# Kernel tuning notes

Measured on AMD Instinct MI355X. Metric: run time of the kernel, lower is better.

## Reference

```python
import jax, jax.numpy as jnp
import numpy as np

C_IN, C_OUT = 64, 32
SD, RFF = 2, 16
RF = 0.05          # receptive_field percentile
TEMP = 1.0
EPS = 1e-8
RFF_STD = 6.0


def setup_inputs() -> dict:
    key = jax.random.key(0)
    ks = jax.random.split(key, 10)
    B_, T, V, Q = 2, 4, 2048, 512
    x = jax.random.normal(ks[0], (B_, T, V, C_IN), dtype=jnp.float32)
    pos = jax.random.uniform(ks[1], (V, SD), dtype=jnp.float32)
    query_pos = jax.random.uniform(ks[2], (Q, SD), dtype=jnp.float32)
    s = 1.0 / np.sqrt(C_IN)
    W_lin = jax.random.uniform(ks[3], (C_IN, C_IN), minval=-s, maxval=s, dtype=jnp.float32)
    b_lin = jax.random.uniform(ks[4], (C_IN,), minval=-s, maxval=s, dtype=jnp.float32)
    Bmat = RFF_STD * jax.random.normal(ks[5], (SD, RFF), dtype=jnp.float32)
    s1 = 1.0 / np.sqrt(32)
    W1 = jax.random.uniform(ks[6], (32, 32), minval=-s1, maxval=s1, dtype=jnp.float32)
    b1 = jax.random.uniform(ks[7], (32,), minval=-s1, maxval=s1, dtype=jnp.float32)
    W2 = jax.random.uniform(ks[8], (C_IN * C_OUT, 32), minval=-s1, maxval=s1, dtype=jnp.float32)
    sf = np.sqrt(3.0 / C_IN)
    filt = jax.random.uniform(ks[9], (C_IN * C_OUT,), minval=-sf, maxval=sf, dtype=jnp.float32)
    bias = jnp.zeros((C_OUT,), dtype=jnp.float32)
    return {"x": x, "pos": pos, "query_pos": query_pos, "W_lin": W_lin, "b_lin": b_lin,
            "Bmat": Bmat, "W1": W1, "b1": b1, "W2": W2, "filt": filt, "bias": bias}


def reference(x, pos, query_pos, W_lin, b_lin, Bmat, W1, b1, W2, filt, bias):
    # pairwise periodic displacement / squared distance
    dist = query_pos[:, None, :] - pos[None, :, :]            # (Q, V, 2)
    dist = (dist + 0.5) % 1.0 - 0.5                           # periodic wrap
    edist = jnp.sum(dist ** 2, axis=-1)                       # (Q, V)
    # quantile threshold -> max neighbourhood size (eager, data-dependent like torch)
    thr = jnp.quantile(edist, RF, axis=-1, keepdims=True)     # linear interpolation, as torch
    K = int(jnp.max(jnp.sum(edist <= thr, axis=-1)))
    _, ind = jax.lax.top_k(-edist, K)                         # (Q, K) nearest neighbours
    # gather per-query neighbour displacements / distances
    d_g = jnp.take_along_axis(dist, ind[..., None], axis=1)   # (Q, K, 2)
    e_g = jnp.take_along_axis(edist, ind, axis=1)[..., None]  # (Q, K, 1)
    e_g = e_g - jnp.min(e_g, axis=-2, keepdims=True)
    e_g = e_g / (jnp.max(e_g, axis=-2, keepdims=True) + EPS)
    k_dist = jax.nn.softmax(-e_g / TEMP, axis=-2)             # (Q, K, 1)
    # random Fourier features + kernel MLP
    proj = 2.0 * jnp.pi * (d_g @ Bmat)                        # (Q, K, 16)
    kfeat = jnp.concatenate([jnp.sin(proj), jnp.cos(proj)], axis=-1)  # (Q, K, 32)
    h = jax.nn.gelu(kfeat @ W1.T + b1, approximate=False)
    ker = (h @ W2.T + filt) * k_dist                          # (Q, K, C_IN*C_OUT)
    ker = ker.reshape(ker.shape[0], ker.shape[1], C_IN, C_OUT)
    # point-wise linear on features, then gather + contract
    xl = x @ W_lin.T + b_lin                                  # (B, T, V, C_IN)
    xg = xl[:, :, ind, :]                                     # (B, T, Q, K, C_IN)
    return jnp.einsum('qvcd,btqvc->btqd', ker, xg) + bias     # (B, T, Q, C_OUT)
```

## Files before the change

### kernel.cpp

```cpp
#include <hip/hip_runtime.h>

#define K_SEL 103
typedef unsigned long long ull_t;
typedef _Float16 f16x8 __attribute__((ext_vector_type(8)));
typedef float f32x4 __attribute__((ext_vector_type(4)));

__global__ __launch_bounds__(512, 6) void klin(const float* __restrict__ x,
                                               const float* __restrict__ W,
                                               const float* __restrict__ b,
                                               _Float16* __restrict__ xlh,
                                               const float* __restrict__ W2,
                                               const float* __restrict__ filt,
                                               _Float16* __restrict__ W2th) {
    __shared__ __align__(16) float Wt[64 * 65];
    const int tid = threadIdx.x;
    const int bb = blockIdx.x;
    if (tid < 264) {
        int t = bb * 264 + tid;
        int d = t & 31;
        int e = t >> 5;
        int c = e & 63;
        int j = e >> 6;
        float v = (j < 32) ? W2[(c * 32 + d) * 32 + j] : filt[c * 32 + d];
        W2th[d * 2112 + e] = (_Float16)v;
    }
    for (int t = tid; t < 4096; t += 512)
        Wt[(t & 63) * 65 + (t >> 6)] = W[t];
    __syncthreads();
    const int i = tid & 63;
    const int sub = tid >> 6;
    const float bi = b[i];
    #pragma unroll
    for (int rr = 0; rr < 2; ++rr) {
        const int r0 = bb * 64 + rr * 32 + sub * 4;
        float acc0 = bi, acc1 = bi, acc2 = bi, acc3 = bi;
        const float* xr = x + (size_t)r0 * 64;
        #pragma unroll 4
        for (int jj = 0; jj < 16; ++jj) {
            float4 v0 = *(const float4*)(xr + 0 * 64 + jj * 4);
            float4 v1 = *(const float4*)(xr + 1 * 64 + jj * 4);
            float4 v2 = *(const float4*)(xr + 2 * 64 + jj * 4);
            float4 v3 = *(const float4*)(xr + 3 * 64 + jj * 4);
            float w0 = Wt[(jj * 4 + 0) * 65 + i];
            float w1 = Wt[(jj * 4 + 1) * 65 + i];
            float w2 = Wt[(jj * 4 + 2) * 65 + i];
            float w3 = Wt[(jj * 4 + 3) * 65 + i];
            acc0 += v0.x * w0 + v0.y * w1 + v0.z * w2 + v0.w * w3;
            acc1 += v1.x * w0 + v1.y * w1 + v1.z * w2 + v1.w * w3;
            acc2 += v2.x * w0 + v2.y * w1 + v2.z * w2 + v2.w * w3;
            acc3 += v3.x * w0 + v3.y * w1 + v3.z * w2 + v3.w * w3;
        }
        xlh[(size_t)(r0 + 0) * 64 + i] = (_Float16)acc0;
        xlh[(size_t)(r0 + 1) * 64 + i] = (_Float16)acc1;
        xlh[(size_t)(r0 + 2) * 64 + i] = (_Float16)acc2;
        xlh[(size_t)(r0 + 3) * 64 + i] = (_Float16)acc3;
    }
}

__global__ __launch_bounds__(512, 4) void kmain(const float* __restrict__ pos,
                                                const float* __restrict__ qpos,
                                                const float* __restrict__ Bmat,
                                                const float* __restrict__ W1,
                                                const float* __restrict__ b1,
                                                const _Float16* __restrict__ xlh,
                                                const _Float16* __restrict__ W2th,
                                                const float* __restrict__ bias,
                                                float* __restrict__ out) {
    __shared__ __align__(16) unsigned char smem[81680];
    _Float16* Hs    = (_Float16*)smem;
    int*      ind   = (int*)(smem + 12288);
    float*    inv_s = (float*)(smem + 12800);
    unsigned char* SG = smem + 12816;

    const int tid = threadIdx.x;
    const int q = blockIdx.x;
    const int lane = tid & 63;
    const int wid = tid >> 6;

    {
        unsigned* ebits   = (unsigned*)(SG);
        unsigned* hist    = (unsigned*)(SG + 8192);
        float*    W1s     = (float*)(SG + 24576);
        float*    b1s     = (float*)(SG + 28672);
        float*    Bm      = (float*)(SG + 28800);
        int*      sel_v   = (int*)(SG + 28928);
        float*    sel_e   = (float*)(SG + 29344);
        ull_t*    bnd     = (ull_t*)(SG + 29760);
        int*      counters= (int*)(SG + 30784);
        int*      info    = (int*)(SG + 30792);
        float*    wred    = (float*)(SG + 30800);
        float*    emax_s  = (float*)(SG + 30832);
        unsigned* wscan   = (unsigned*)(SG + 30836);

        for (int t = tid; t < 1024; t += 512) W1s[t] = W1[t];
        if (tid < 32) { b1s[tid] = b1[tid]; Bm[tid] = Bmat[tid]; }
        if (tid < 2)  counters[tid] = 0;
        for (int t = tid; t < 1024; t += 512) ((uint4*)hist)[t] = make_uint4(0, 0, 0, 0);
        const float qp0 = qpos[q * 2 + 0];
        const float qp1 = qpos[q * 2 + 1];
        __syncthreads();

        float lmin = 1e30f;
        for (int v = tid; v < 2048; v += 512) {
            float2 p = ((const float2*)pos)[v];
            float d0 = qp0 - p.x;
            float d1 = qp1 - p.y;
            d0 += 0.5f; d0 -= floorf(d0); d0 -= 0.5f;
            d1 += 0.5f; d1 -= floorf(d1); d1 -= 0.5f;
            float e = d0 * d0 + d1 * d1;
            ebits[v] = __float_as_uint(e);
            lmin = fminf(lmin, e);
            int bb2 = (int)(e * 8192.0f); bb2 = (bb2 > 4095) ? 4095 : bb2;
            atomicAdd(&hist[bb2], 1u);
        }
        #pragma unroll
        for (int off = 32; off > 0; off >>= 1)
            lmin = fminf(lmin, __shfl_xor(lmin, off, 64));
        if (lane == 0) wred[wid] = lmin;
        __syncthreads();
        float e_min = wred[0];
        #pragma unroll
        for (int w2 = 1; w2 < 8; ++w2) e_min = fminf(e_min, wred[w2]);

        unsigned lsum = 0;
        #pragma unroll
        for (int i = 0; i < 8; ++i) lsum += hist[tid * 8 + i];
        unsigned vq = lsum;
        #pragma unroll
        for (int off = 1; off < 64; off <<= 1) {
            unsigned n = __shfl_up(vq, off, 64);
            if (lane >= off) vq += n;
        }
        if (lane == 63) wscan[wid] = vq;
        __syncthreads();
        unsigned base = 0;
        for (int w2 = 0; w2 < wid; ++w2) base += wscan[w2];
        unsigned cum = base + vq - lsum;
        #pragma unroll
        for (int i = 0; i < 8; ++i) {
            unsigned cnt = hist[tid * 8 + i];
            if (cum <= 102u && 102u < cum + cnt) { info[0] = tid * 8 + i; info[1] = (int)cum; }
            cum += cnt;
        }
        __syncthreads();
        const int Bstar = info[0];
        const int L = info[1];
        const int need = K_SEL - L;

        {
            f16x8 z = {0, 0, 0, 0, 0, 0, 0, 0};
            for (int t = tid; t < 768; t += 512) ((f16x8*)Hs)[t] = z;
        }
        for (int v = tid; v < 2048; v += 512) {
            unsigned bb2 = ebits[v];
            float e = __uint_as_float(bb2);
            int bin = (int)(e * 8192.0f); bin = (bin > 4095) ? 4095 : bin;
            if (bin < Bstar) {
                int s2 = atomicAdd(&counters[0], 1);
                sel_v[s2] = v; sel_e[s2] = e;
            } else if (bin == Bstar) {
                int s2 = atomicAdd(&counters[1], 1);
                if (s2 < 128) bnd[s2] = (((ull_t)bb2) << 32) | (unsigned)v;
            }
        }
        __syncthreads();
        {
            int nb = counters[1]; if (nb > 128) nb = 128;
            if (tid < nb) {
                ull_t my = bnd[tid];
                int rank = 0;
                for (int i = 0; i < nb; ++i) rank += (bnd[i] < my);
                if (rank < need) {
                    sel_v[L + rank] = (int)(unsigned)(my & 0xffffffffull);
                    sel_e[L + rank] = __uint_as_float((unsigned)(my >> 32));
                }
                if (rank == need - 1)
                    emax_s[0] = __uint_as_float((unsigned)(my >> 32));
            }
        }
        __syncthreads();

        const float denom = (emax_s[0] - e_min) + 1e-8f;
        float w = 0.0f;
        if (tid < K_SEL) {
            w = __expf(-(sel_e[tid] - e_min) / denom);
            sel_e[tid] = w;
        }
        float sw = w;
        #pragma unroll
        for (int off = 32; off > 0; off >>= 1)
            sw += __shfl_xor(sw, off, 64);
        if (lane == 0) wred[wid] = sw;
        __syncthreads();
        if (tid == 0) {
            float tot = 0.0f;
            #pragma unroll
            for (int w2 = 0; w2 < 8; ++w2) tot += wred[w2];
            inv_s[0] = 1.0f / tot;
        }

        if (tid < 4 * K_SEL) {
            const int k = tid >> 2;
            const int io = (tid & 3) * 8;
            const int v = sel_v[k];
            const float wk = sel_e[k];
            float2 p = ((const float2*)pos)[v];
            float d0 = qp0 - p.x;
            float d1 = qp1 - p.y;
            d0 += 0.5f; d0 -= floorf(d0); d0 -= 0.5f;
            d1 += 0.5f; d1 -= floorf(d1); d1 -= 0.5f;
            float kf[32];
            #pragma unroll
            for (int f = 0; f < 16; ++f) {
                float t = d0 * Bm[f] + d1 * Bm[16 + f];
                float r = t - rintf(t);
                kf[f]      = __builtin_amdgcn_sinf(r);
                kf[16 + f] = __builtin_amdgcn_cosf(r);
            }
            #pragma unroll
            for (int i = io; i < io + 8; ++i) {
                float pre = b1s[i];
                #pragma unroll
                for (int jf = 0; jf < 32; ++jf) pre += kf[jf] * W1s[i * 32 + jf];
                float g = 0.5f * pre * (1.0f + erff(pre * 0.70710678118654752f));
                Hs[i * 128 + k] = (_Float16)(g * wk);
            }
            if (io == 0) {
                Hs[32 * 128 + k] = (_Float16)wk;
                ind[k] = v;
            }
        }
        __syncthreads();
        if (tid < 128 - K_SEL) ind[K_SEL + tid] = ind[tid];
    }

    {
        const int h   = wid >> 2;
        const int cq  = wid & 3;
        const int n0 = lane & 15;
        const int quad = lane >> 4;

        _Float16* Xg  = (_Float16*)SG;
        _Float16* Zh8 = (_Float16*)(SG + 35072);
        float* red    = (float*)SG;

        f16x8 afr[4][3];
        #pragma unroll
        for (int ks = 0; ks < 4; ++ks)
            #pragma unroll
            for (int r = 0; r < 3; ++r)
                afr[ks][r] = *(const f16x8*)(Hs + (r * 16 + n0) * 128 + ks * 32 + quad * 8);
        const float it = inv_s[0];
        const int e0f = wid * 32 + quad * 8;
        f16x8 pf0 = *(const f16x8*)(W2th + (size_t)(0 * 16 + n0) * 2112 + e0f);
        f16x8 pf1 = *(const f16x8*)(W2th + (size_t)(1 * 16 + n0) * 2112 + e0f);
        __syncthreads();

        int g_k[4], g_oct[4], g_h[4];
        #pragma unroll
        for (int i = 0; i < 4; ++i) {
            int t = tid + i * 512;
            g_h[i] = t >> 10;
            g_k[i] = (t >> 3) & 127;
            g_oct[i] = t & 7;
        }

        {
            f16x8 v0[4];
            #pragma unroll
            for (int i = 0; i < 4; ++i)
                v0[i] = *(const f16x8*)(xlh + ((size_t)g_h[i] * 2048 + ind[g_k[i]]) * 64 + g_oct[i] * 8);
            #pragma unroll
            for (int i = 0; i < 4; ++i) {
                int base = g_h[i] * 8768 + g_oct[i] * 1096 + g_k[i];
                #pragma unroll
                for (int jj = 0; jj < 8; ++jj) Xg[base + 136 * jj] = v0[i][jj];
            }
        }
        __syncthreads();

        const int cA = cq * 16 + n0;
        const int cswz = h * 8768 + cA * 136 + ((cA >> 3) << 3);

        #pragma unroll
        for (int p = 0; p < 4; ++p) {
            f16x8 vn[4];
            if (p < 3) {
                #pragma unroll
                for (int i = 0; i < 4; ++i)
                    vn[i] = *(const f16x8*)(xlh + ((size_t)(2 * (p + 1) + g_h[i]) * 2048 + ind[g_k[i]]) * 64 + g_oct[i] * 8);
            }
            f32x4 Dz[3];
            #pragma unroll
            for (int r = 0; r < 3; ++r) Dz[r] = (f32x4){0.f, 0.f, 0.f, 0.f};
            #pragma unroll
            for (int ks = 0; ks < 4; ++ks) {
                f16x8 bfr = *(const f16x8*)(&Xg[cswz + ks * 32 + quad * 8]);
                #pragma unroll
                for (int r = 0; r < 3; ++r)
                    Dz[r] = __builtin_amdgcn_mfma_f32_16x16x32_f16(afr[ks][r], bfr, Dz[r], 0, 0, 0);
            }
            __syncthreads();
            const int bt = 2 * p + h;
            #pragma unroll
            for (int r = 0; r < 3; ++r)
                #pragma unroll
                for (int reg = 0; reg < 4; ++reg) {
                    int j = r * 16 + quad * 4 + reg;
                    if (j < 33) Zh8[bt * 2112 + j * 64 + cA] = (_Float16)Dz[r][reg];
                }
            if (p < 3) {
                #pragma unroll
                for (int i = 0; i < 4; ++i) {
                    int base = g_h[i] * 8768 + g_oct[i] * 1096 + g_k[i];
                    #pragma unroll
                    for (int jj = 0; jj < 8; ++jj) Xg[base + 136 * jj] = vn[i][jj];
                }
                __syncthreads();
            }
        }
        __syncthreads();

        f32x4 D2[2][2];
        #pragma unroll
        for (int pp = 0; pp < 2; ++pp)
            #pragma unroll
            for (int dt = 0; dt < 2; ++dt) D2[pp][dt] = (f32x4){0.f, 0.f, 0.f, 0.f};
        {
            f16x8 a2 = {0, 0, 0, 0, 0, 0, 0, 0};
            if (n0 < 8) a2 = *(const f16x8*)(&Zh8[n0 * 2112 + e0f]);
            D2[0][0] = __builtin_amdgcn_mfma_f32_16x16x32_f16(a2, pf0, D2[0][0], 0, 0, 0);
            D2[0][1] = __builtin_amdgcn_mfma_f32_16x16x32_f16(a2, pf1, D2[0][1], 0, 0, 0);
        }
        int pp = 1;
        #pragma unroll 2
        for (int s = wid + 8; s < 66; s += 8) {
            const int e0 = s * 32 + quad * 8;
            f16x8 a2 = {0, 0, 0, 0, 0, 0, 0, 0};
            if (n0 < 8) a2 = *(const f16x8*)(&Zh8[n0 * 2112 + e0]);
            #pragma unroll
            for (int dt = 0; dt < 2; ++dt) {
                f16x8 bfr = *(const f16x8*)(W2th + (size_t)(dt * 16 + n0) * 2112 + e0);
                D2[pp][dt] = __builtin_amdgcn_mfma_f32_16x16x32_f16(a2, bfr, D2[pp][dt], 0, 0, 0);
            }
            pp ^= 1;
        }
        #pragma unroll
        for (int dt = 0; dt < 2; ++dt)
            D2[0][dt] = D2[0][dt] + D2[1][dt];

        if (quad < 2) {
            #pragma unroll
            for (int dt = 0; dt < 2; ++dt)
                #pragma unroll
                for (int reg = 0; reg < 4; ++reg)
                    red[((wid * 2 + dt) * 8 + quad * 4 + reg) * 16 + n0] = D2[0][dt][reg];
        }
        __syncthreads();
        if (tid < 256) {
            const int bt = tid >> 5;
            const int d = tid & 31;
            const int dt = d >> 4;
            const int dn = d & 15;
            float s = 0.0f;
            #pragma unroll
            for (int w2 = 0; w2 < 8; ++w2)
                s += red[((w2 * 2 + dt) * 8 + bt) * 16 + dn];
            out[((size_t)bt * 512 + q) * 32 + d] = bias[d] + it * s;
        }
    }
}

extern "C" void kernel_launch(void* const* d_in, const int* in_sizes, int n_in,
                              void* d_out, int out_size, void* d_ws, size_t ws_size,
                              hipStream_t stream) {
    const float* x     = (const float*)d_in[0];
    const float* pos   = (const float*)d_in[1];
    const float* qpos  = (const float*)d_in[2];
    const float* W_lin = (const float*)d_in[3];
    const float* b_lin = (const float*)d_in[4];
    const float* Bmat  = (const float*)d_in[5];
    const float* W1    = (const float*)d_in[6];
    const float* b1    = (const float*)d_in[7];
    const float* W2    = (const float*)d_in[8];
    const float* filt  = (const float*)d_in[9];
    const float* bias  = (const float*)d_in[10];
    float* out = (float*)d_out;

    float* ws = (float*)d_ws;
    _Float16* xlh  = (_Float16*)ws;
    _Float16* W2th = (_Float16*)(ws + 524288);

    klin<<<256, 512, 0, stream>>>(x, W_lin, b_lin, xlh, W2, filt, W2th);
    kmain<<<512, 512, 0, stream>>>(pos, qpos, Bmat, W1, b1, xlh, W2th, bias, out);
}
```

Measured before the change: 115.7 us.

## Fuse linear prologue into main kernel with global atomic counter barrier

Merges the point-wise linear/W2-transpose kernel into the main per-query kernel. Each of the 512 blocks computes a slice of xlh and W2th, then increments a global counter, and waits on it only just before gathering xlh. This removes one kernel launch and lets the distance/top-k phase overlap with the linear prologue. In exchange it adds a memset and a spin-wait grid barrier, which relies on all 512 blocks being co-resident (512 threads each, about 80KB LDS) or it can deadlock.

```diff
diff --git a/kernel.cpp b/kernel.cpp
--- a/kernel.cpp
+++ b/kernel.cpp
@@ -5,34 +5,50 @@
 typedef _Float16 f16x8 __attribute__((ext_vector_type(8)));
 typedef float f32x4 __attribute__((ext_vector_type(4)));
 
-__global__ __launch_bounds__(512, 6) void klin(const float* __restrict__ x,
+__global__ __launch_bounds__(512, 4) void kall(const float* __restrict__ pos,
+                                               const float* __restrict__ qpos,
+                                               const float* __restrict__ Bmat,
+                                               const float* __restrict__ W1,
+                                               const float* __restrict__ b1,
+                                               const float* __restrict__ x,
                                                const float* __restrict__ W,
                                                const float* __restrict__ b,
                                                _Float16* __restrict__ xlh,
                                                const float* __restrict__ W2,
                                                const float* __restrict__ filt,
-                                               _Float16* __restrict__ W2th) {
-    __shared__ __align__(16) float Wt[64 * 65];
+                                               _Float16* __restrict__ W2th,
+                                               const float* __restrict__ bias,
+                                               unsigned* __restrict__ ctr,
+                                               float* __restrict__ out) {
+    __shared__ __align__(16) unsigned char smem[81680];
+    _Float16* Hs    = (_Float16*)smem;
+    int*      ind   = (int*)(smem + 12288);
+    float*    inv_s = (float*)(smem + 12800);
+    unsigned char* SG = smem + 12816;
+
     const int tid = threadIdx.x;
-    const int bb = blockIdx.x;
-    if (tid < 264) {
-        int t = bb * 264 + tid;
-        int d = t & 31;
-        int e = t >> 5;
-        int c = e & 63;
-        int j = e >> 6;
-        float v = (j < 32) ? W2[(c * 32 + d) * 32 + j] : filt[c * 32 + d];
-        W2th[d * 2112 + e] = (_Float16)v;
-    }
-    for (int t = tid; t < 4096; t += 512)
-        Wt[(t & 63) * 65 + (t >> 6)] = W[t];
-    __syncthreads();
-    const int i = tid & 63;
-    const int sub = tid >> 6;
-    const float bi = b[i];
-    #pragma unroll
-    for (int rr = 0; rr < 2; ++rr) {
-        const int r0 = bb * 64 + rr * 32 + sub * 4;
+    const int q = blockIdx.x;
+    const int lane = tid & 63;
+    const int wid = tid >> 6;
+
+    {
+        float* Wt = (float*)SG;
+        if (tid < 132) {
+            int t = q * 132 + tid;
+            int d = t & 31;
+            int e = t >> 5;
+            int c = e & 63;
+            int j = e >> 6;
+            float v = (j < 32) ? W2[(c * 32 + d) * 32 + j] : filt[c * 32 + d];
+            W2th[d * 2112 + e] = (_Float16)v;
+        }
+        for (int t = tid; t < 4096; t += 512)
+            Wt[(t & 63) * 65 + (t >> 6)] = W[t];
+        __syncthreads();
+        const int i = tid & 63;
+        const int sub = tid >> 6;
+        const float bi = b[i];
+        const int r0 = q * 32 + sub * 4;
         float acc0 = bi, acc1 = bi, acc2 = bi, acc3 = bi;
         const float* xr = x + (size_t)r0 * 64;
         #pragma unroll 4
@@ -54,28 +70,11 @@
         xlh[(size_t)(r0 + 1) * 64 + i] = (_Float16)acc1;
         xlh[(size_t)(r0 + 2) * 64 + i] = (_Float16)acc2;
         xlh[(size_t)(r0 + 3) * 64 + i] = (_Float16)acc3;
+        __syncthreads();
+        if (tid == 0)
+            __hip_atomic_fetch_add(ctr, 1u, __ATOMIC_RELEASE,
+                                   __HIP_MEMORY_SCOPE_AGENT);
     }
-}
-
-__global__ __launch_bounds__(512, 4) void kmain(const float* __restrict__ pos,
-                                                const float* __restrict__ qpos,
-                                                const float* __restrict__ Bmat,
-                                                const float* __restrict__ W1,
-                                                const float* __restrict__ b1,
-                                                const _Float16* __restrict__ xlh,
-                                                const _Float16* __restrict__ W2th,
-                                                const float* __restrict__ bias,
-                                                float* __restrict__ out) {
-    __shared__ __align__(16) unsigned char smem[81680];
-    _Float16* Hs    = (_Float16*)smem;
-    int*      ind   = (int*)(smem + 12288);
-    float*    inv_s = (float*)(smem + 12800);
-    unsigned char* SG = smem + 12816;
-
-    const int tid = threadIdx.x;
-    const int q = blockIdx.x;
-    const int lane = tid & 63;
-    const int wid = tid >> 6;
 
     {
         unsigned* ebits   = (unsigned*)(SG);
@@ -251,10 +250,17 @@
             for (int r = 0; r < 3; ++r)
                 afr[ks][r] = *(const f16x8*)(Hs + (r * 16 + n0) * 128 + ks * 32 + quad * 8);
         const float it = inv_s[0];
+
+        if (lane == 0) {
+            while (__hip_atomic_load(ctr, __ATOMIC_ACQUIRE,
+                                     __HIP_MEMORY_SCOPE_AGENT) < 512u)
+                __builtin_amdgcn_s_sleep(8);
+        }
+        __syncthreads();
+
         const int e0f = wid * 32 + quad * 8;
         f16x8 pf0 = *(const f16x8*)(W2th + (size_t)(0 * 16 + n0) * 2112 + e0f);
         f16x8 pf1 = *(const f16x8*)(W2th + (size_t)(1 * 16 + n0) * 2112 + e0f);
-        __syncthreads();
 
         int g_k[4], g_oct[4], g_h[4];
         #pragma unroll
@@ -390,7 +396,9 @@
     float* ws = (float*)d_ws;
     _Float16* xlh  = (_Float16*)ws;
     _Float16* W2th = (_Float16*)(ws + 524288);
-
-    klin<<<256, 512, 0, stream>>>(x, W_lin, b_lin, xlh, W2, filt, W2th);
-    kmain<<<512, 512, 0, stream>>>(pos, qpos, Bmat, W1, b1, xlh, W2th, bias, out);
+    unsigned* ctr  = (unsigned*)(ws + 558080);
+
+    hipMemsetAsync(ctr, 0, sizeof(unsigned), stream);
+    kall<<<512, 512, 0, stream>>>(pos, qpos, Bmat, W1, b1, x, W_lin, b_lin,
+                                  xlh, W2, filt, W2th, bias, ctr, out);
 }
```

New measurement: 139.7 us. 1.21x slower.
